# Kernel tuning notes

Measured on AMD Instinct MI355X. Metric: run time of the kernel, lower is better.

The kernel has to match this reference:

```python
import jax, jax.numpy as jnp
import numpy as np

B, T, C, H = 2, 2048, 1024, 16
HD = C // H  # head dim = 64


def setup_inputs() -> dict:
    key = jax.random.key(0)
    k1, k2, k3 = jax.random.split(key, 3)
    scale_in = 1.0 / np.sqrt(C)
    x = jax.random.normal(k1, (B, T, C), dtype=jnp.float32)
    w_qkv = jax.random.normal(k2, (C, 3 * C), dtype=jnp.float32) * scale_in
    b_qkv = jnp.zeros((3 * C,), dtype=jnp.float32)
    w_out = jax.random.normal(k3, (C, C), dtype=jnp.float32) * scale_in
    b_out = jnp.zeros((C,), dtype=jnp.float32)
    return {"x": x, "w_qkv": w_qkv, "b_qkv": b_qkv, "w_out": w_out, "b_out": b_out}


def reference(x, w_qkv, b_qkv, w_out, b_out):
    Bq, Tq, Cq = x.shape
    qkv = x @ w_qkv + b_qkv                       # [B,T,3C]
    q, k, v = jnp.split(qkv, 3, axis=-1)          # each [B,T,C]
    # [B,T,C] -> [B,H,T,HD]
    q = q.reshape(Bq, Tq, H, HD).transpose(0, 2, 1, 3)
    k = k.reshape(Bq, Tq, H, HD).transpose(0, 2, 1, 3)
    v = v.reshape(Bq, Tq, H, HD).transpose(0, 2, 1, 3)
    scale = 1.0 / np.sqrt(HD)
    scores = jnp.einsum("bhqd,bhkd->bhqk", q, k) * scale  # [B,H,T,T]
    causal = jnp.tril(jnp.ones((Tq, Tq), dtype=bool))
    scores = jnp.where(causal[None, None], scores, jnp.finfo(scores.dtype).min)
    attn = jax.nn.softmax(scores, axis=-1)
    y = jnp.einsum("bhqk,bhkd->bhqd", attn, v)    # [B,H,T,HD]
    y = y.transpose(0, 2, 1, 3).reshape(Bq, Tq, Cq)
    return y @ w_out + b_out
```

## Files before the change

kernel.cpp:

```cpp
#include <hip/hip_runtime.h>
#include <hip/hip_bf16.h>


#define B_ 2
#define T_ 2048
#define C_ 1024
#define H_ 16
#define HD_ 64
#define M_ (B_ * T_)
#define N3_ (3 * C_)
#define QSCALE 0.18033688f

typedef __attribute__((ext_vector_type(8))) short short8;
typedef __attribute__((ext_vector_type(4))) short short4v;
typedef __attribute__((ext_vector_type(4))) float floatx4;

__device__ __forceinline__ unsigned short f2b(float f) {
    __hip_bfloat16 h = __float2bfloat16(f);
    return *reinterpret_cast<unsigned short*>(&h);
}

__device__ __forceinline__ float fexp2(float x) {
#if __has_builtin(__builtin_amdgcn_exp2f)
    return __builtin_amdgcn_exp2f(x);
#else
    return exp2f(x);
#endif
}

__device__ __forceinline__ void glds16(const void* g, void* l) {
    __builtin_amdgcn_global_load_lds(
        (const __attribute__((address_space(1))) void*)g,
        (__attribute__((address_space(3))) void*)l, 16, 0, 0);
}

__global__ __launch_bounds__(256) void prep(
    const float* __restrict__ x, const float* __restrict__ w_qkv,
    const float* __restrict__ w_out, unsigned short* __restrict__ xb,
    unsigned short* __restrict__ wt1, unsigned short* __restrict__ wt2) {
    __shared__ float t[64][33];
    const int bi = blockIdx.x;
    const int tid = threadIdx.x;
    if (bi < 4096) {
        int i = (bi * 256 + tid) * 4;
        float4 v = *reinterpret_cast<const float4*>(x + i);
        short4v s;
        s[0] = (short)f2b(v.x); s[1] = (short)f2b(v.y);
        s[2] = (short)f2b(v.z); s[3] = (short)f2b(v.w);
        *reinterpret_cast<short4v*>(xb + i) = s;
        return;
    }
    const float* src; unsigned short* dst; int n0, k0, N;
    if (bi < 4096 + 1536) {
        int u = bi - 4096;
        src = w_qkv; dst = wt1; N = N3_;
        k0 = (u & 15) * 64; n0 = (u >> 4) * 32;
    } else {
        int u = bi - (4096 + 1536);
        src = w_out; dst = wt2; N = C_;
        k0 = (u & 15) * 64; n0 = (u >> 4) * 32;
    }
    const int tx = tid & 31, ty = tid >> 5;
#pragma unroll
    for (int i = 0; i < 8; i++)
        t[ty + i * 8][tx] = src[(size_t)(k0 + ty + i * 8) * N + n0 + tx];
    __syncthreads();
    const int row = tid >> 3;
    const int kp  = (tid & 7) * 8;
    short8 o;
#pragma unroll
    for (int j = 0; j < 8; j++) o[j] = (short)f2b(t[kp + j][row]);
    *reinterpret_cast<short8*>(&dst[(size_t)(n0 + row) * C_ + k0 + kp]) = o;
}

template<int EPI, int BN>
__global__ __launch_bounds__(256) void gemm_glds(
    const unsigned short* __restrict__ A, const unsigned short* __restrict__ Bt,
    const float* __restrict__ bias, void* __restrict__ Cp,
    unsigned short* __restrict__ kfbp, unsigned short* __restrict__ vfbp,
    int M, int N, int K) {
    constexpr int NI = BN / 32;
    __shared__ __align__(16) unsigned short Al[128 * 64];
    __shared__ __align__(16) unsigned short Bl[BN * 64];

    const int tid  = threadIdx.x;
    const int lane = tid & 63;
    const int w    = tid >> 6;
    const int c16  = lane & 15;
    const int quad = lane >> 4;
    const int NT  = N / BN;
    const int pe  = NT >> 3;
    const int xcd = blockIdx.x & 7;
    const int ii  = blockIdx.x >> 3;
    const int n0  = (xcd * pe + ii % pe) * BN;
    const int m0  = (ii / pe) * 128;
    const int wm = (w >> 1) * 64;
    const int wn = (w & 1) * (BN / 2);

    floatx4 acc[4][NI] = {};

    const int srow = lane >> 3;
    const int sch  = ((lane & 7) ^ srow) * 8;
    const unsigned short* ag = A + (size_t)(m0 + w * 32 + srow) * K + sch;
    const unsigned short* bg = Bt + (size_t)(n0 + w * (BN / 4) + srow) * K + sch;

    const int s7 = c16 & 7;

    for (int k0 = 0; k0 < K; k0 += 64) {
        __syncthreads();
#pragma unroll
        for (int i = 0; i < 4; i++)
            glds16(ag + k0 + (size_t)(i * 8) * K, &Al[(w * 32 + i * 8) * 64]);
#pragma unroll
        for (int i = 0; i < BN / 32; i++)
            glds16(bg + k0 + (size_t)(i * 8) * K,
                   &Bl[(w * (BN / 4) + i * 8) * 64]);
        __syncthreads();

        short8 af[4][2], bf[NI][2];
#pragma unroll
        for (int im = 0; im < 4; im++)
#pragma unroll
            for (int kk = 0; kk < 2; kk++)
                af[im][kk] = *reinterpret_cast<const short8*>(
                    &Al[(wm + im * 16 + c16) * 64 + ((kk * 4 + quad) ^ s7) * 8]);
#pragma unroll
        for (int in = 0; in < NI; in++)
#pragma unroll
            for (int kk = 0; kk < 2; kk++)
                bf[in][kk] = *reinterpret_cast<const short8*>(
                    &Bl[(wn + in * 16 + c16) * 64 + ((kk * 4 + quad) ^ s7) * 8]);
#pragma unroll
        for (int im = 0; im < 4; im++)
#pragma unroll
            for (int in = 0; in < NI; in++)
#pragma unroll
                for (int kk = 0; kk < 2; kk++)
                    acc[im][in] = __builtin_amdgcn_mfma_f32_16x16x32_bf16(
                        af[im][kk], bf[in][kk], acc[im][in], 0, 0, 0);
    }

    const int ncol = n0 + wn;
    float bv[NI];
#pragma unroll
    for (int in = 0; in < NI; in++) bv[in] = bias[ncol + in * 16 + c16];

    if (EPI == 0) {
        float* C = (float*)Cp;
#pragma unroll
        for (int im = 0; im < 4; im++)
#pragma unroll
            for (int r = 0; r < 4; r++) {
                int row = m0 + wm + im * 16 + quad * 4 + r;
#pragma unroll
                for (int in = 0; in < NI; in++)
                    C[(size_t)row * N + ncol + in * 16 + c16] =
                        acc[im][in][r] + bv[in];
            }
    } else {
        if (ncol < C_) {
            unsigned short* qb = (unsigned short*)Cp;
#pragma unroll
            for (int im = 0; im < 4; im++)
#pragma unroll
                for (int r = 0; r < 4; r++) {
                    int row = m0 + wm + im * 16 + quad * 4 + r;
#pragma unroll
                    for (int in = 0; in < NI; in++)
                        qb[(size_t)row * C_ + ncol + in * 16 + c16] =
                            f2b((acc[im][in][r] + bv[in]) * QSCALE);
                }
        } else if (ncol < 2 * C_) {
#pragma unroll
            for (int im = 0; im < 4; im++) {
                int row0 = m0 + wm + im * 16 + quad * 4;
                int b    = row0 >> 11;
                int key  = row0 & (T_ - 1);
                int chunk = key >> 6;
                int kk    = key & 63;
                int wsd   = kk >> 5;
                int subd  = (kk >> 4) & 1;
                int c16d  = kk & 15;
#pragma unroll
                for (int in = 0; in < NI; in++) {
                    int dfull = ncol - C_ + in * 16 + c16;
                    int hh = dfull >> 6;
                    int d  = dfull & 63;
                    size_t base =
                        ((size_t)((b * 16 + hh) * 32 + chunk)) * 4096 +
                        (wsd * 4 + subd * 2 + (d >> 5)) * 512 +
                        (((d >> 3) & 3) * 16 + c16d) * 8 + (d & 7);
#pragma unroll
                    for (int r = 0; r < 4; r++)
                        kfbp[base + (size_t)r * 8] =
                            f2b(acc[im][in][r] + bv[in]);
                }
            }
        } else {
#pragma unroll
            for (int im = 0; im < 4; im++) {
                int row0 = m0 + wm + im * 16 + quad * 4;
                int b    = row0 >> 11;
                int key  = row0 & (T_ - 1);
                int chunk = key >> 6;
                int kk    = key & 63;
                int wsd   = kk >> 5;
                int qd    = (kk >> 2) & 3;
                int jb    = (kk & 16) ? 4 : 0;
#pragma unroll
                for (int in = 0; in < NI; in++) {
                    int dfull = ncol - 2 * C_ + in * 16 + c16;
                    int hh = dfull >> 6;
                    int d  = dfull & 63;
                    short4v sv;
#pragma unroll
                    for (int r = 0; r < 4; r++)
                        sv[r] = (short)f2b(acc[im][in][r] + bv[in]);
                    *reinterpret_cast<short4v*>(
                        &vfbp[((size_t)((b * 16 + hh) * 32 + chunk)) * 4096 +
                              (wsd * 4 + (d >> 4)) * 512 +
                              (qd * 16 + (d & 15)) * 8 + jb]) = sv;
                }
            }
        }
    }
}

#define ATTN_CHUNK(MASKED, kb, kcp, vcp)                                      \
{                                                                             \
    short8 kf00 = *reinterpret_cast<const short8*>((kcp));                    \
    short8 kf01 = *reinterpret_cast<const short8*>((kcp) + 512);              \
    short8 kf10 = *reinterpret_cast<const short8*>((kcp) + 1024);             \
    short8 kf11 = *reinterpret_cast<const short8*>((kcp) + 1536);             \
    short8 vf[4];                                                             \
    _Pragma("unroll")                                                         \
    for (int dt = 0; dt < 4; dt++)                                            \
        vf[dt] = *reinterpret_cast<const short8*>((vcp) + dt * 512);          \
    short8 pf[2];                                                             \
    _Pragma("unroll")                                                         \
    for (int qt = 0; qt < 2; qt++) {                                          \
        floatx4 s0 = __builtin_amdgcn_mfma_f32_16x16x32_bf16(                 \
            kf00, af[qt][0], z, 0, 0, 0);                                     \
        s0 = __builtin_amdgcn_mfma_f32_16x16x32_bf16(                         \
            kf01, af[qt][1], s0, 0, 0, 0);                                    \
        floatx4 s1 = __builtin_amdgcn_mfma_f32_16x16x32_bf16(                 \
            kf10, af[qt][0], z, 0, 0, 0);                                     \
        s1 = __builtin_amdgcn_mfma_f32_16x16x32_bf16(                         \
            kf11, af[qt][1], s1, 0, 0, 0);                                    \
        short8 p8;                                                            \
        _Pragma("unroll")                                                     \
        for (int r = 0; r < 4; r++) {                                         \
            float p0, p1;                                                     \
            if (MASKED) {                                                     \
                int key0 = (kb) + ws * 32 + quad * 4 + r;                     \
                int qr = q0 + wq * 32 + qt * 16 + c16;                        \
                p0 = (key0 <= qr) ? fexp2(s0[r]) : 0.f;                       \
                p1 = (key0 + 16 <= qr) ? fexp2(s1[r]) : 0.f;                  \
            } else {                                                          \
                p0 = fexp2(s0[r]);                                            \
                p1 = fexp2(s1[r]);                                            \
            }                                                                 \
            p8[r] = (short)f2b(p0);                                           \
            p8[4 + r] = (short)f2b(p1);                                       \
        }                                                                     \
        pf[qt] = p8;                                                          \
    }                                                                         \
    _Pragma("unroll")                                                         \
    for (int qt = 0; qt < 2; qt++)                                            \
        O1[qt] = __builtin_amdgcn_mfma_f32_16x16x32_bf16(                     \
            pf[qt], ones, O1[qt], 0, 0, 0);                                   \
    _Pragma("unroll")                                                         \
    for (int dt = 0; dt < 4; dt++)                                            \
        _Pragma("unroll")                                                     \
        for (int qt = 0; qt < 2; qt++)                                        \
            O[qt][dt] = __builtin_amdgcn_mfma_f32_16x16x32_bf16(              \
                pf[qt], vf[dt], O[qt][dt], 0, 0, 0);                          \
}

__global__ __launch_bounds__(256, 3) void attn_mfma(
    const unsigned short* __restrict__ qk,
    const unsigned short* __restrict__ kfb,
    const unsigned short* __restrict__ vfb,
    unsigned short* __restrict__ y) {
    __shared__ __align__(16) float Of[4096];
    __shared__ __align__(16) float Lb[1024];

    const int tid  = threadIdx.x;
    const int lane = tid & 63;
    const int w    = tid >> 6;
    const int wq   = w & 1;
    const int ws   = w >> 1;
    const int c16  = lane & 15;
    const int quad = lane >> 4;
    const int bh = blockIdx.x & 31;
    const int t  = 31 - (blockIdx.x >> 5);
    const int b  = bh >> 4;
    const int h  = bh & 15;
    const int q0 = t * 64;
    const int nch = t + 1;

    const unsigned short* qrow = qk + (size_t)b * T_ * C_ + h * HD_;
    const unsigned short* kfp = kfb + ((size_t)bh * 32) * 4096 + ws * 2048 + lane * 8;
    const unsigned short* vfp = vfb + ((size_t)bh * 32) * 4096 + ws * 2048 + lane * 8;

    short8 af[2][2];
#pragma unroll
    for (int qt = 0; qt < 2; qt++)
#pragma unroll
        for (int hh = 0; hh < 2; hh++)
            af[qt][hh] = *reinterpret_cast<const short8*>(
                qrow + (size_t)(q0 + wq * 32 + qt * 16 + c16) * C_ +
                hh * 32 + quad * 8);

    floatx4 O[2][4] = {};
    floatx4 O1[2] = {};
    const floatx4 z = {0.f, 0.f, 0.f, 0.f};
    short8 ones;
#pragma unroll
    for (int j = 0; j < 8; j++) ones[j] = (short)0x3F80;

    for (int c = 0; c < nch; c++) {
        const int kb = c * 64;
        const unsigned short* kcp = kfp + (size_t)c * 4096;
        const unsigned short* vcp = vfp + (size_t)c * 4096;
        if (c + 1 < nch) {
            ATTN_CHUNK(0, kb, kcp, vcp)
        } else if (!(wq == 0 && ws == 1)) {
            ATTN_CHUNK(1, kb, kcp, vcp)
        }
    }

    if (ws) {
#pragma unroll
        for (int qt = 0; qt < 2; qt++) {
#pragma unroll
            for (int dt = 0; dt < 4; dt++)
                *reinterpret_cast<floatx4*>(
                    &Of[wq * 2048 + qt * 1024 + dt * 256 + lane * 4]) = O[qt][dt];
            *reinterpret_cast<floatx4*>(
                &Lb[wq * 512 + qt * 256 + lane * 4]) = O1[qt];
        }
    }
    __syncthreads();
    if (ws == 0) {
#pragma unroll
        for (int qt = 0; qt < 2; qt++) {
#pragma unroll
            for (int dt = 0; dt < 4; dt++)
                O[qt][dt] += *reinterpret_cast<const floatx4*>(
                    &Of[wq * 2048 + qt * 1024 + dt * 256 + lane * 4]);
            floatx4 lr = O1[qt] + *reinterpret_cast<const floatx4*>(
                    &Lb[wq * 512 + qt * 256 + lane * 4]);

#pragma unroll
            for (int dt = 0; dt < 4; dt++)
#pragma unroll
                for (int r = 0; r < 4; r++) {
                    float val = O[qt][dt][r] / fmaxf(lr[r], 1e-30f);
                    y[((size_t)b * T_ + q0 + wq * 32 + qt * 16 + quad * 4 + r)
                          * C_ + h * HD_ + dt * 16 + c16] = f2b(val);
                }
        }
    }
}

extern "C" void kernel_launch(void* const* d_in, const int* in_sizes, int n_in,
                              void* d_out, int out_size, void* d_ws, size_t ws_size,
                              hipStream_t stream) {
    const float* x     = (const float*)d_in[0];
    const float* w_qkv = (const float*)d_in[1];
    const float* b_qkv = (const float*)d_in[2];
    const float* w_out = (const float*)d_in[3];
    const float* b_out = (const float*)d_in[4];
    float* out = (float*)d_out;

    unsigned short* qb  = (unsigned short*)d_ws;
    unsigned short* kfb = qb + (size_t)M_ * C_;
    unsigned short* vfb = kfb + (size_t)32 * 32 * 4096;
    unsigned short* yb  = vfb + (size_t)32 * 32 * 4096;
    unsigned short* wt1 = yb + (size_t)M_ * C_;
    unsigned short* wt2 = wt1 + (size_t)N3_ * C_;
    unsigned short* xb  = wt2 + (size_t)C_ * C_;

    prep<<<4096 + 1536 + 512, 256, 0, stream>>>(x, w_qkv, w_out, xb, wt1, wt2);

    gemm_glds<1, 128><<<(N3_ / 128) * (M_ / 128), 256, 0, stream>>>(
        xb, wt1, b_qkv, qb, kfb, vfb, M_, N3_, C_);

    attn_mfma<<<B_ * H_ * 32, 256, 0, stream>>>(qb, kfb, vfb, yb);

    gemm_glds<0, 64><<<(C_ / 64) * (M_ / 128), 256, 0, stream>>>(
        yb, wt2, b_out, out, nullptr, nullptr, M_, C_, C_);
}
```

Measured before the change: 172.2 us.

## Double-buffer K/V fragment loads in attention loop and widen x conversion

Result: faster. 161.4 us (-6.2%).

```diff
diff --git a/kernel.cpp b/kernel.cpp
--- a/kernel.cpp
+++ b/kernel.cpp
@@ -41,22 +41,25 @@
     __shared__ float t[64][33];
     const int bi = blockIdx.x;
     const int tid = threadIdx.x;
-    if (bi < 4096) {
-        int i = (bi * 256 + tid) * 4;
-        float4 v = *reinterpret_cast<const float4*>(x + i);
-        short4v s;
-        s[0] = (short)f2b(v.x); s[1] = (short)f2b(v.y);
-        s[2] = (short)f2b(v.z); s[3] = (short)f2b(v.w);
-        *reinterpret_cast<short4v*>(xb + i) = s;
+    if (bi < 2048) {
+        int i = (bi * 256 + tid) * 8;
+        float4 v0 = *reinterpret_cast<const float4*>(x + i);
+        float4 v1 = *reinterpret_cast<const float4*>(x + i + 4);
+        short8 s;
+        s[0] = (short)f2b(v0.x); s[1] = (short)f2b(v0.y);
+        s[2] = (short)f2b(v0.z); s[3] = (short)f2b(v0.w);
+        s[4] = (short)f2b(v1.x); s[5] = (short)f2b(v1.y);
+        s[6] = (short)f2b(v1.z); s[7] = (short)f2b(v1.w);
+        *reinterpret_cast<short8*>(xb + i) = s;
         return;
     }
     const float* src; unsigned short* dst; int n0, k0, N;
-    if (bi < 4096 + 1536) {
-        int u = bi - 4096;
+    if (bi < 2048 + 1536) {
+        int u = bi - 2048;
         src = w_qkv; dst = wt1; N = N3_;
         k0 = (u & 15) * 64; n0 = (u >> 4) * 32;
     } else {
-        int u = bi - (4096 + 1536);
+        int u = bi - (2048 + 1536);
         src = w_out; dst = wt2; N = C_;
         k0 = (u & 15) * 64; n0 = (u >> 4) * 32;
     }
@@ -226,27 +229,33 @@
     }
 }
 
-#define ATTN_CHUNK(MASKED, kb, kcp, vcp)                                      \
+#define ATTN_LOADF(K0, K1, K2, K3, V0, V1, V2, V3, cc)                        \
 {                                                                             \
-    short8 kf00 = *reinterpret_cast<const short8*>((kcp));                    \
-    short8 kf01 = *reinterpret_cast<const short8*>((kcp) + 512);              \
-    short8 kf10 = *reinterpret_cast<const short8*>((kcp) + 1024);             \
-    short8 kf11 = *reinterpret_cast<const short8*>((kcp) + 1536);             \
-    short8 vf[4];                                                             \
-    _Pragma("unroll")                                                         \
-    for (int dt = 0; dt < 4; dt++)                                            \
-        vf[dt] = *reinterpret_cast<const short8*>((vcp) + dt * 512);          \
-    short8 pf[2];                                                             \
+    const unsigned short* kcp_ = kfp + (size_t)(cc) * 4096;                   \
+    const unsigned short* vcp_ = vfp + (size_t)(cc) * 4096;                   \
+    K0 = *reinterpret_cast<const short8*>(kcp_);                              \
+    K1 = *reinterpret_cast<const short8*>(kcp_ + 512);                        \
+    K2 = *reinterpret_cast<const short8*>(kcp_ + 1024);                       \
+    K3 = *reinterpret_cast<const short8*>(kcp_ + 1536);                       \
+    V0 = *reinterpret_cast<const short8*>(vcp_);                              \
+    V1 = *reinterpret_cast<const short8*>(vcp_ + 512);                        \
+    V2 = *reinterpret_cast<const short8*>(vcp_ + 1024);                       \
+    V3 = *reinterpret_cast<const short8*>(vcp_ + 1536);                       \
+}
+
+#define ATTN_COMPUTE(MASKED, kb, K0, K1, K2, K3, V0, V1, V2, V3)              \
+{                                                                             \
+    short8 pf0, pf1;                                                          \
     _Pragma("unroll")                                                         \
     for (int qt = 0; qt < 2; qt++) {                                          \
         floatx4 s0 = __builtin_amdgcn_mfma_f32_16x16x32_bf16(                 \
-            kf00, af[qt][0], z, 0, 0, 0);                                     \
+            K0, af[qt][0], z, 0, 0, 0);                                       \
         s0 = __builtin_amdgcn_mfma_f32_16x16x32_bf16(                         \
-            kf01, af[qt][1], s0, 0, 0, 0);                                    \
+            K1, af[qt][1], s0, 0, 0, 0);                                      \
         floatx4 s1 = __builtin_amdgcn_mfma_f32_16x16x32_bf16(                 \
-            kf10, af[qt][0], z, 0, 0, 0);                                     \
+            K2, af[qt][0], z, 0, 0, 0);                                       \
         s1 = __builtin_amdgcn_mfma_f32_16x16x32_bf16(                         \
-            kf11, af[qt][1], s1, 0, 0, 0);                                    \
+            K3, af[qt][1], s1, 0, 0, 0);                                      \
         short8 p8;                                                            \
         _Pragma("unroll")                                                     \
         for (int r = 0; r < 4; r++) {                                         \
@@ -263,21 +272,21 @@
             p8[r] = (short)f2b(p0);                                           \
             p8[4 + r] = (short)f2b(p1);                                       \
         }                                                                     \
-        pf[qt] = p8;                                                          \
+        if (qt == 0) pf0 = p8; else pf1 = p8;                                 \
     }                                                                         \
-    _Pragma("unroll")                                                         \
-    for (int qt = 0; qt < 2; qt++)                                            \
-        O1[qt] = __builtin_amdgcn_mfma_f32_16x16x32_bf16(                     \
-            pf[qt], ones, O1[qt], 0, 0, 0);                                   \
-    _Pragma("unroll")                                                         \
-    for (int dt = 0; dt < 4; dt++)                                            \
-        _Pragma("unroll")                                                     \
-        for (int qt = 0; qt < 2; qt++)                                        \
-            O[qt][dt] = __builtin_amdgcn_mfma_f32_16x16x32_bf16(              \
-                pf[qt], vf[dt], O[qt][dt], 0, 0, 0);                          \
-}
-
-__global__ __launch_bounds__(256, 3) void attn_mfma(
+    O1[0] = __builtin_amdgcn_mfma_f32_16x16x32_bf16(pf0, ones, O1[0], 0, 0, 0); \
+    O1[1] = __builtin_amdgcn_mfma_f32_16x16x32_bf16(pf1, ones, O1[1], 0, 0, 0); \
+    O[0][0] = __builtin_amdgcn_mfma_f32_16x16x32_bf16(pf0, V0, O[0][0], 0, 0, 0); \
+    O[1][0] = __builtin_amdgcn_mfma_f32_16x16x32_bf16(pf1, V0, O[1][0], 0, 0, 0); \
+    O[0][1] = __builtin_amdgcn_mfma_f32_16x16x32_bf16(pf0, V1, O[0][1], 0, 0, 0); \
+    O[1][1] = __builtin_amdgcn_mfma_f32_16x16x32_bf16(pf1, V1, O[1][1], 0, 0, 0); \
+    O[0][2] = __builtin_amdgcn_mfma_f32_16x16x32_bf16(pf0, V2, O[0][2], 0, 0, 0); \
+    O[1][2] = __builtin_amdgcn_mfma_f32_16x16x32_bf16(pf1, V2, O[1][2], 0, 0, 0); \
+    O[0][3] = __builtin_amdgcn_mfma_f32_16x16x32_bf16(pf0, V3, O[0][3], 0, 0, 0); \
+    O[1][3] = __builtin_amdgcn_mfma_f32_16x16x32_bf16(pf1, V3, O[1][3], 0, 0, 0); \
+}
+
+__global__ __launch_bounds__(256, 2) void attn_mfma(
     const unsigned short* __restrict__ qk,
     const unsigned short* __restrict__ kfb,
     const unsigned short* __restrict__ vfb,
@@ -319,15 +328,29 @@
 #pragma unroll
     for (int j = 0; j < 8; j++) ones[j] = (short)0x3F80;
 
-    for (int c = 0; c < nch; c++) {
-        const int kb = c * 64;
-        const unsigned short* kcp = kfp + (size_t)c * 4096;
-        const unsigned short* vcp = vfp + (size_t)c * 4096;
+    short8 A0, A1, A2, A3, AV0, AV1, AV2, AV3;
+    short8 B0, B1, B2, B3, BV0, BV1, BV2, BV3;
+    ATTN_LOADF(A0, A1, A2, A3, AV0, AV1, AV2, AV3, 0);
+    int c = 0;
+    for (;;) {
         if (c + 1 < nch) {
-            ATTN_CHUNK(0, kb, kcp, vcp)
-        } else if (!(wq == 0 && ws == 1)) {
-            ATTN_CHUNK(1, kb, kcp, vcp)
+            ATTN_LOADF(B0, B1, B2, B3, BV0, BV1, BV2, BV3, c + 1);
+            ATTN_COMPUTE(0, c * 64, A0, A1, A2, A3, AV0, AV1, AV2, AV3);
+        } else {
+            if (!(wq == 0 && ws == 1))
+                ATTN_COMPUTE(1, c * 64, A0, A1, A2, A3, AV0, AV1, AV2, AV3);
+            break;
         }
+        c++;
+        if (c + 1 < nch) {
+            ATTN_LOADF(A0, A1, A2, A3, AV0, AV1, AV2, AV3, c + 1);
+            ATTN_COMPUTE(0, c * 64, B0, B1, B2, B3, BV0, BV1, BV2, BV3);
+        } else {
+            if (!(wq == 0 && ws == 1))
+                ATTN_COMPUTE(1, c * 64, B0, B1, B2, B3, BV0, BV1, BV2, BV3);
+            break;
+        }
+        c++;
     }
 
     if (ws) {
@@ -382,7 +405,7 @@
     unsigned short* wt2 = wt1 + (size_t)N3_ * C_;
     unsigned short* xb  = wt2 + (size_t)C_ * C_;
 
-    prep<<<4096 + 1536 + 512, 256, 0, stream>>>(x, w_qkv, w_out, xb, wt1, wt2);
+    prep<<<2048 + 1536 + 512, 256, 0, stream>>>(x, w_qkv, w_out, xb, wt1, wt2);
 
     gemm_glds<1, 128><<<(N3_ / 128) * (M_ / 128), 256, 0, stream>>>(
         xb, wt1, b_qkv, qb, kfb, vfb, M_, N3_, C_);
```
